# Optimization experiments

Measured on AMD Instinct MI355X. Metric: run time of the kernel, lower is better.

## Reference

```python
import jax, jax.numpy as jnp
import numpy as np

B, C, T, F, D, S = 16, 128, 64, 128, 2, 62  # batch, w_dim, seq_in, feat, dilation, seq_out


def setup_inputs() -> dict:
    key = jax.random.key(0)
    ks = jax.random.split(key, 9)
    x = jax.random.normal(ks[0], (B, C, T, F), dtype=jnp.float32)
    # depthwise (2,1) dilated conv params: weight[c, tap]
    w_tanh = jax.random.normal(ks[1], (C, 2), dtype=jnp.float32) * 0.5
    b_tanh = jax.random.normal(ks[2], (C,), dtype=jnp.float32) * 0.1
    w_sig = jax.random.normal(ks[3], (C, 2), dtype=jnp.float32) * 0.5
    b_sig = jax.random.normal(ks[4], (C,), dtype=jnp.float32) * 0.1
    # depthwise 1x1 out conv: one scalar weight + bias per channel
    w_out = jax.random.normal(ks[5], (C,), dtype=jnp.float32) * 0.5
    b_out = jax.random.normal(ks[6], (C,), dtype=jnp.float32) * 0.1
    # residual Linear(seq_in=T -> seq_out=S)
    w_res = jax.random.normal(ks[7], (S, T), dtype=jnp.float32) * (1.0 / np.sqrt(T))
    b_res = jax.random.normal(ks[8], (S,), dtype=jnp.float32) * 0.1
    return {"x": x, "w_tanh": w_tanh, "b_tanh": b_tanh, "w_sig": w_sig,
            "b_sig": b_sig, "w_out": w_out, "b_out": b_out,
            "w_res": w_res, "b_res": b_res, "dilation": D}


def reference(x, w_tanh, b_tanh, w_sig, b_sig, w_out, b_out, w_res, b_res, dilation):
    d = dilation
    # depthwise dilated conv, kernel (2,1): out[t] = w[0]*x[t] + w[1]*x[t+d]
    x0 = x[:, :, : x.shape[2] - d, :]          # [B,C,S,F]
    x1 = x[:, :, d:, :]                         # [B,C,S,F]
    cexp = lambda v: v[None, :, None, None]
    xt = x0 * cexp(w_tanh[:, 0]) + x1 * cexp(w_tanh[:, 1]) + cexp(b_tanh)
    xs = x0 * cexp(w_sig[:, 0]) + x1 * cexp(w_sig[:, 1]) + cexp(b_sig)
    gate = jnp.tanh(xt) * jax.nn.sigmoid(xs)    # [B,C,S,F]
    # residual: Linear over T, output laid out as [B,C,S,F]
    res = jnp.einsum('bctf,st->bcsf', x, w_res) + b_res[None, None, :, None]
    # depthwise 1x1 conv
    out = (gate + res) * cexp(w_out) + cexp(b_out)
    return out
```

## Files before the change

kernel.cpp:

```cpp
#include <hip/hip_runtime.h>


typedef __attribute__((ext_vector_type(8)))  short short8;
typedef __attribute__((ext_vector_type(4)))  float f32x4;
typedef __attribute__((ext_vector_type(4)))  int   i32x4;
typedef __attribute__((ext_vector_type(2)))  float f32x2;

constexpr int Bc = 16, Cc = 128, Tc = 64, Fc = 128, Sc = 62, DIL = 2;
constexpr int LDSW = 130;

__device__ inline unsigned cvt_pk_bf16(float lo, float hi) {
    unsigned r;
    asm("v_cvt_pk_bf16_f32 %0, %1, %2" : "=v"(r) : "v"(lo), "v"(hi));
    return r;
}

__global__ void prep_kernel(const float* __restrict__ w_res,
                            const float* __restrict__ b_res,
                            void* __restrict__ ws)
{
    const int tid = threadIdx.x;
    i32x4* wa = (i32x4*)ws;
    float* brs = (float*)((char*)ws + 8192);
    for (int u = tid; u < 512; u += 256) {
        const int frag = u >> 6, lane = u & 63;
        const int rt = frag >> 1, kt = frag & 1;
        const int row = 16 * rt + (lane & 15);
        const int g = lane >> 4;
        unsigned p[4];
#pragma unroll
        for (int q = 0; q < 4; ++q) {
            float lo = 0.f, hi = 0.f;
            if (row < Sc) {
                const int k = 32 * kt + 8 * g + 2 * q;
                lo = w_res[row * Tc + k];
                hi = w_res[row * Tc + k + 1];
            }
            p[q] = cvt_pk_bf16(lo, hi);
        }
        wa[u] = i32x4{(int)p[0], (int)p[1], (int)p[2], (int)p[3]};
    }
    if (tid < 64) brs[tid] = (tid < Sc) ? b_res[tid] : 0.f;
}

__global__ __launch_bounds__(256, 4)
void gated_mfma_kernel(const float* __restrict__ x,
                       const float* __restrict__ w_tanh,
                       const float* __restrict__ b_tanh,
                       const float* __restrict__ w_sig,
                       const float* __restrict__ b_sig,
                       const float* __restrict__ w_out,
                       const float* __restrict__ b_out,
                       const void* __restrict__ ws,
                       float* __restrict__ out)
{
    __shared__ float lds[Tc * LDSW];

    const int bc   = blockIdx.x;
    const int c    = bc & (Cc - 1);
    const int tid  = threadIdx.x;
    const int lane = tid & 63;
    const int w    = tid >> 6;
    const int g    = lane >> 4;
    const int r16  = lane & 15;

    const float wt0 = w_tanh[2 * c + 0], wt1 = w_tanh[2 * c + 1], bt = b_tanh[c];
    const float ws0 = w_sig[2 * c + 0],  ws1 = w_sig[2 * c + 1],  bs = b_sig[c];
    const float wo  = w_out[c],          bo  = b_out[c];

    const float* xp = x + (size_t)bc * (Tc * Fc);
#pragma unroll
    for (int i = 0; i < 8; ++i) {
        const int o   = tid * 4 + i * 1024;
        const int t   = o >> 7;
        const int col = o & 127;
        const f32x4 v = *(const f32x4*)(xp + o);
        float* d = lds + t * LDSW + col;
        *(f32x2*)(d + 0) = f32x2{v.x, v.y};
        *(f32x2*)(d + 2) = f32x2{v.z, v.w};
    }
    __syncthreads();

    const short8* wa = (const short8*)ws;
    short8 A[4][2];
#pragma unroll
    for (int rt = 0; rt < 4; ++rt)
#pragma unroll
        for (int kt = 0; kt < 2; ++kt)
            A[rt][kt] = wa[(rt * 2 + kt) * 64 + lane];

    const float* brs = (const float*)((const char*)ws + 8192);
    f32x4 acc[4][2];
#pragma unroll
    for (int rt = 0; rt < 4; ++rt) {
        const f32x4 bv = *(const f32x4*)(brs + 16 * rt + 4 * g);
        acc[rt][0] = bv;
        acc[rt][1] = bv;
    }

    const int col0 = 32 * w + r16;
#pragma unroll
    for (int kt = 0; kt < 2; ++kt) {
        short8 Bf[2];
#pragma unroll
        for (int ct = 0; ct < 2; ++ct) {
            const float* bp = lds + (32 * kt + 8 * g) * LDSW + col0 + 16 * ct;
            const unsigned p0 = cvt_pk_bf16(bp[0 * LDSW], bp[1 * LDSW]);
            const unsigned p1 = cvt_pk_bf16(bp[2 * LDSW], bp[3 * LDSW]);
            const unsigned p2 = cvt_pk_bf16(bp[4 * LDSW], bp[5 * LDSW]);
            const unsigned p3 = cvt_pk_bf16(bp[6 * LDSW], bp[7 * LDSW]);
            Bf[ct] = __builtin_bit_cast(short8, i32x4{(int)p0, (int)p1, (int)p2, (int)p3});
        }
#pragma unroll
        for (int rt = 0; rt < 4; ++rt)
#pragma unroll
            for (int ct = 0; ct < 2; ++ct)
                acc[rt][ct] = __builtin_amdgcn_mfma_f32_16x16x32_bf16(
                    A[rt][kt], Bf[ct], acc[rt][ct], 0, 0, 0);
    }

    float* op = out + (size_t)bc * (Sc * Fc);
#pragma unroll
    for (int rt = 0; rt < 4; ++rt) {
#pragma unroll
        for (int reg = 0; reg < 4; ++reg) {
            const int row = 16 * rt + 4 * g + reg;
            if (row < Sc) {
#pragma unroll
                for (int ct = 0; ct < 2; ++ct) {
                    const int col = col0 + 16 * ct;
                    const float x0 = lds[row * LDSW + col];
                    const float x1 = lds[(row + DIL) * LDSW + col];
                    const float xt  = fmaf(x0, wt0, fmaf(x1, wt1, bt));
                    const float xsg = fmaf(x0, ws0, fmaf(x1, ws1, bs));
                    const float e2 = __expf(2.0f * xt);
                    const float th = (e2 - 1.0f) * __builtin_amdgcn_rcpf(e2 + 1.0f);
                    const float sg = __builtin_amdgcn_rcpf(1.0f + __expf(-xsg));
                    const float v  = fmaf(th * sg + acc[rt][ct][reg], wo, bo);
                    op[row * Fc + col] = v;
                }
            }
        }
    }
}

extern "C" void kernel_launch(void* const* d_in, const int* in_sizes, int n_in,
                              void* d_out, int out_size, void* d_ws, size_t ws_size,
                              hipStream_t stream)
{
    const float* x      = (const float*)d_in[0];
    const float* w_tanh = (const float*)d_in[1];
    const float* b_tanh = (const float*)d_in[2];
    const float* w_sig  = (const float*)d_in[3];
    const float* b_sig  = (const float*)d_in[4];
    const float* w_out  = (const float*)d_in[5];
    const float* b_out  = (const float*)d_in[6];
    const float* w_res  = (const float*)d_in[7];
    const float* b_res  = (const float*)d_in[8];

    float* out = (float*)d_out;

    prep_kernel<<<1, 256, 0, stream>>>(w_res, b_res, d_ws);
    gated_mfma_kernel<<<Bc * Cc, 256, 0, stream>>>(
        x, w_tanh, b_tanh, w_sig, b_sig, w_out, b_out, d_ws, out);
}
```

Baseline: 33.61 us.

## Fold weight prep into main kernel and reuse LDS rows in gate epilogue

Removes the separate single-block prep kernel launch, so each block loads w_res/b_res from global memory and converts them to bf16 fragments itself. The global weight loads are issued before the barrier so they overlap the LDS fill. The epilogue now loads six LDS rows once per 4-row group, sharing them between the x0 and x1 taps. It also merges the tanh and sigmoid reciprocals into one rcp. The cost is redundant per-block weight loads and conversions, plus a slightly larger LDS buffer (66 rows), which adds nothing since rows 64-65 are only read for rows that are skipped.

```diff
diff --git a/kernel.cpp b/kernel.cpp
--- a/kernel.cpp
+++ b/kernel.cpp
@@ -7,40 +7,13 @@
 typedef __attribute__((ext_vector_type(2)))  float f32x2;
 
 constexpr int Bc = 16, Cc = 128, Tc = 64, Fc = 128, Sc = 62, DIL = 2;
-constexpr int LDSW = 130;
+constexpr int LDSW    = 130;
+constexpr int LDSROWS = 66;
 
 __device__ inline unsigned cvt_pk_bf16(float lo, float hi) {
     unsigned r;
     asm("v_cvt_pk_bf16_f32 %0, %1, %2" : "=v"(r) : "v"(lo), "v"(hi));
     return r;
-}
-
-__global__ void prep_kernel(const float* __restrict__ w_res,
-                            const float* __restrict__ b_res,
-                            void* __restrict__ ws)
-{
-    const int tid = threadIdx.x;
-    i32x4* wa = (i32x4*)ws;
-    float* brs = (float*)((char*)ws + 8192);
-    for (int u = tid; u < 512; u += 256) {
-        const int frag = u >> 6, lane = u & 63;
-        const int rt = frag >> 1, kt = frag & 1;
-        const int row = 16 * rt + (lane & 15);
-        const int g = lane >> 4;
-        unsigned p[4];
-#pragma unroll
-        for (int q = 0; q < 4; ++q) {
-            float lo = 0.f, hi = 0.f;
-            if (row < Sc) {
-                const int k = 32 * kt + 8 * g + 2 * q;
-                lo = w_res[row * Tc + k];
-                hi = w_res[row * Tc + k + 1];
-            }
-            p[q] = cvt_pk_bf16(lo, hi);
-        }
-        wa[u] = i32x4{(int)p[0], (int)p[1], (int)p[2], (int)p[3]};
-    }
-    if (tid < 64) brs[tid] = (tid < Sc) ? b_res[tid] : 0.f;
 }
 
 __global__ __launch_bounds__(256, 4)
@@ -51,10 +24,11 @@
                        const float* __restrict__ b_sig,
                        const float* __restrict__ w_out,
                        const float* __restrict__ b_out,
-                       const void* __restrict__ ws,
+                       const float* __restrict__ w_res,
+                       const float* __restrict__ b_res,
                        float* __restrict__ out)
 {
-    __shared__ float lds[Tc * LDSW];
+    __shared__ float lds[LDSROWS * LDSW];
 
     const int bc   = blockIdx.x;
     const int c    = bc & (Cc - 1);
@@ -79,24 +53,44 @@
         *(f32x2*)(d + 0) = f32x2{v.x, v.y};
         *(f32x2*)(d + 2) = f32x2{v.z, v.w};
     }
-    __syncthreads();
 
-    const short8* wa = (const short8*)ws;
     short8 A[4][2];
 #pragma unroll
-    for (int rt = 0; rt < 4; ++rt)
+    for (int rt = 0; rt < 4; ++rt) {
+        const int row = 16 * rt + r16;
+        const bool ok = row < Sc;
+        const float* wr = w_res + row * Tc + 8 * g;
 #pragma unroll
-        for (int kt = 0; kt < 2; ++kt)
-            A[rt][kt] = wa[(rt * 2 + kt) * 64 + lane];
+        for (int kt = 0; kt < 2; ++kt) {
+            f32x4 v0 = f32x4{0.f, 0.f, 0.f, 0.f};
+            f32x4 v1 = f32x4{0.f, 0.f, 0.f, 0.f};
+            if (ok) {
+                v0 = *(const f32x4*)(wr + 32 * kt);
+                v1 = *(const f32x4*)(wr + 32 * kt + 4);
+            }
+            const unsigned p0 = cvt_pk_bf16(v0.x, v0.y);
+            const unsigned p1 = cvt_pk_bf16(v0.z, v0.w);
+            const unsigned p2 = cvt_pk_bf16(v1.x, v1.y);
+            const unsigned p3 = cvt_pk_bf16(v1.z, v1.w);
+            A[rt][kt] = __builtin_bit_cast(short8,
+                          i32x4{(int)p0, (int)p1, (int)p2, (int)p3});
+        }
+    }
 
-    const float* brs = (const float*)((const char*)ws + 8192);
     f32x4 acc[4][2];
 #pragma unroll
     for (int rt = 0; rt < 4; ++rt) {
-        const f32x4 bv = *(const f32x4*)(brs + 16 * rt + 4 * g);
+        f32x4 bv;
+#pragma unroll
+        for (int j = 0; j < 4; ++j) {
+            const int idx = 16 * rt + 4 * g + j;
+            bv[j] = b_res[idx < Sc ? idx : Sc - 1];
+        }
         acc[rt][0] = bv;
         acc[rt][1] = bv;
     }
+
+    __syncthreads();
 
     const int col0 = 32 * w + r16;
 #pragma unroll
@@ -122,24 +116,34 @@
     float* op = out + (size_t)bc * (Sc * Fc);
 #pragma unroll
     for (int rt = 0; rt < 4; ++rt) {
+        const int r0 = 16 * rt + 4 * g;
 #pragma unroll
-        for (int reg = 0; reg < 4; ++reg) {
-            const int row = 16 * rt + 4 * g + reg;
-            if (row < Sc) {
-#pragma unroll
-                for (int ct = 0; ct < 2; ++ct) {
-                    const int col = col0 + 16 * ct;
-                    const float x0 = lds[row * LDSW + col];
-                    const float x1 = lds[(row + DIL) * LDSW + col];
-                    const float xt  = fmaf(x0, wt0, fmaf(x1, wt1, bt));
-                    const float xsg = fmaf(x0, ws0, fmaf(x1, ws1, bs));
-                    const float e2 = __expf(2.0f * xt);
-                    const float th = (e2 - 1.0f) * __builtin_amdgcn_rcpf(e2 + 1.0f);
-                    const float sg = __builtin_amdgcn_rcpf(1.0f + __expf(-xsg));
-                    const float v  = fmaf(th * sg + acc[rt][ct][reg], wo, bo);
-                    op[row * Fc + col] = v;
-                }
+        for (int ct = 0; ct < 2; ++ct) {
+            const int col = col0 + 16 * ct;
+            const float* bp = lds + r0 * LDSW + col;
+            const float t0 = bp[0 * LDSW];
+            const float t1 = bp[1 * LDSW];
+            const float t2 = bp[2 * LDSW];
+            const float t3 = bp[3 * LDSW];
+            const float t4 = bp[4 * LDSW];
+            const float t5 = bp[5 * LDSW];
+
+#define GATE_OUT(reg, xa, xb)                                                     \
+            if (r0 + (reg) < Sc) {                                                \
+                const float xt  = fmaf((xa), wt0, fmaf((xb), wt1, bt));           \
+                const float xsg = fmaf((xa), ws0, fmaf((xb), ws1, bs));           \
+                const float e2  = __expf(2.0f * xt);                              \
+                const float em  = __expf(-xsg);                                   \
+                const float gate = (e2 - 1.0f) *                                  \
+                    __builtin_amdgcn_rcpf((e2 + 1.0f) * (1.0f + em));             \
+                op[(r0 + (reg)) * Fc + col] =                                     \
+                    fmaf(gate + acc[rt][ct][reg], wo, bo);                        \
             }
+            GATE_OUT(0, t0, t2)
+            GATE_OUT(1, t1, t3)
+            GATE_OUT(2, t2, t4)
+            GATE_OUT(3, t3, t5)
+#undef GATE_OUT
         }
     }
 }
@@ -160,7 +164,6 @@
 
     float* out = (float*)d_out;
 
-    prep_kernel<<<1, 256, 0, stream>>>(w_res, b_res, d_ws);
     gated_mfma_kernel<<<Bc * Cc, 256, 0, stream>>>(
-        x, w_tanh, b_tanh, w_sig, b_sig, w_out, b_out, d_ws, out);
+        x, w_tanh, b_tanh, w_sig, b_sig, w_out, b_out, w_res, b_res, out);
 }
```

Result: no change. 33.62 us (+0.0%).
